# Kernel optimization log

Measured on AMD Instinct MI355X. Metric: run time of the kernel, lower is better.

## Reference

```python
import jax, jax.numpy as jnp
import numpy as np

# Problem sizes (see shape_source)
C = 4096                      # sparse matrix is C x C
NUMEL = C * C                 # 16,777,216
S = 3355443                   # round(NUMEL * 0.2) sampled gradient entries
R = 1048576                   # result_quantity (top-k buffer size)
DECAY = 0.95                  # decay_constant
FRAC = S / float(NUMEL)       # fractional_sparsity (mask_active=False branch)


def setup_inputs() -> dict:
    key = jax.random.key(0)
    k1, k2, k3, k4 = jax.random.split(key, 4)
    # Sampled linear indices into the C x C grid (forward: torch.randint(0, numel, [S]))
    sample_index = jax.random.randint(k1, (S,), 0, NUMEL, dtype=jnp.int32)
    # Steady-state buffer of (row, col) pairs and their running gradient magnitudes
    result_index = jax.random.randint(k2, (R, 2), 0, C, dtype=jnp.int32)
    result_value = jax.random.uniform(k3, (R,), dtype=jnp.float32)
    # Incoming gradient on the sampled accumulator entries
    gradient = jax.random.normal(k4, (S,), dtype=jnp.float32)
    return {
        "sample_index": sample_index,
        "result_index": result_index,
        "result_value": result_value,
        "gradient": gradient,
    }


def reference(sample_index, result_index, result_value, gradient):
    """Faithful JAX version of StochasticSubSampler's backward-hook update:
    decay the stored buffer, take |gradient| on the new samples, coalesce
    duplicated (row, col) entries by summation, then keep the top-R values.
    Returns (new_result_index [R,2] int32, new_result_value [R] float32)."""
    adj_decay = 1.0 - FRAC * (1.0 - DECAY)  # adjusted decay constant

    # Linearized keys for coalescing. sample_index is already row*C + col.
    samp_keys = sample_index
    res_keys = result_index[:, 0] * C + result_index[:, 1]
    keys = jnp.concatenate([samp_keys, res_keys])               # [K]
    vals = jnp.concatenate([jnp.abs(gradient), adj_decay * result_value])  # [K]
    K = keys.shape[0]

    # Coalesce: sum values that share the same (row, col) key.
    uniq, inv = jnp.unique(keys, size=K, fill_value=-1, return_inverse=True)
    summed = jax.ops.segment_sum(vals, inv, num_segments=K)     # [K]
    counts = jax.ops.segment_sum(jnp.ones_like(vals), inv, num_segments=K)
    neg = jnp.finfo(jnp.float32).min
    summed = jnp.where(counts > 0, summed, neg)  # mask padded unique slots

    # Descending sort + top-R selection (argsort(-v)[:R] in the original).
    top_vals, top_pos = jax.lax.top_k(summed, R)
    top_keys = uniq[top_pos]
    new_index = jnp.stack([top_keys // C, top_keys % C], axis=-1)  # [R, 2]
    return new_index, top_vals
```

## Files before the change

### kernel.cpp

```cpp
#include <hip/hip_runtime.h>
#include <stdint.h>

#define CDIM   4096
#define S_N    3355443
#define R_N    1048576
#define N1     (S_N + R_N)
#define TILE   4096
#define NTILES ((N1 + TILE - 1) / TILE)
#define NPAD   (NTILES * TILE)
#define NSB    (NPAD / 256)
#define PAD_KEY 0xFFFFFFu
#define PAD_VAL 0xFFFFFFFFu

static __device__ __forceinline__ unsigned blockScanExcl(unsigned v, unsigned t,
                                                         unsigned* lw, unsigned* tot){
  unsigned lane = t & 63u, w = t >> 6;
  unsigned x = v;
  #pragma unroll
  for (int off = 1; off < 64; off <<= 1){
    unsigned y = __shfl_up(x, off, 64);
    if (lane >= (unsigned)off) x += y;
  }
  if (lane == 63u) lw[w] = x;
  __syncthreads();
  unsigned woff = 0;
  for (unsigned i = 0; i < w; i++) woff += lw[i];
  *tot = lw[0] + lw[1] + lw[2] + lw[3];
  __syncthreads();
  return x + woff - v;
}

__global__ __launch_bounds__(256) void k_build(const int* __restrict__ sidx,
                                               const int* __restrict__ ridx,
                                               const float* __restrict__ rval,
                                               const float* __restrict__ grad,
                                               uint64_t* __restrict__ A){
  unsigned i = blockIdx.x * 256u + threadIdx.x;
  uint32_t key, vb;
  if (i < S_N){
    key = (uint32_t)sidx[i];
    vb  = __float_as_uint(fabsf(grad[i]));
  } else if (i < N1){
    unsigned j = i - S_N;
    key = (uint32_t)(ridx[2u*j] * CDIM + ridx[2u*j + 1u]);
    const float ADJF = (float)(1.0 - (3355443.0 / 16777216.0) * (1.0 - 0.95));
    vb = __float_as_uint(ADJF * rval[j]);
  } else {
    key = PAD_KEY; vb = PAD_VAL;
  }
  A[i] = ((uint64_t)key << 32) | (uint64_t)vb;
}

__global__ __launch_bounds__(256) void k_hist(const uint64_t* __restrict__ in, unsigned shift,
                                              unsigned* __restrict__ gh){
  __shared__ unsigned h[256];
  unsigned t = threadIdx.x;
  h[t] = 0; __syncthreads();
  size_t base = (size_t)blockIdx.x * TILE;
  #pragma unroll
  for (int r = 0; r < 16; r++){
    uint64_t e = in[base + (size_t)r*256 + t];
    atomicAdd(&h[(unsigned)((e >> shift) & 0xFF)], 1u);
  }
  __syncthreads();
  gh[t * NTILES + blockIdx.x] = h[t];
}

__global__ __launch_bounds__(256) void k_scanrows(unsigned* __restrict__ gh,
                                                  unsigned* __restrict__ dtot){
  __shared__ unsigned lw[4];
  unsigned d = blockIdx.x, t = threadIdx.x;
  unsigned carry = 0;
  for (unsigned base = 0; base < NTILES; base += 256){
    unsigned i = base + t;
    unsigned v = (i < NTILES) ? gh[d * NTILES + i] : 0u;
    unsigned tot;
    unsigned e = blockScanExcl(v, t, lw, &tot);
    if (i < NTILES) gh[d * NTILES + i] = e + carry;
    carry += tot;
  }
  if (t == 0) dtot[d] = carry;
}

template <bool FINAL>
__device__ __forceinline__ void scatter_body(const uint64_t* __restrict__ in,
                                             uint64_t* __restrict__ out,
                                             float* __restrict__ fout,
                                             unsigned shift,
                                             const unsigned* __restrict__ gh,
                                             const unsigned* __restrict__ dtot){
  __shared__ unsigned wrun[4*256];
  __shared__ unsigned gput[256];
  __shared__ unsigned lw[4];
  __shared__ uint64_t stage[TILE];
  unsigned t = threadIdx.x, lane = t & 63u, w = t >> 6;
  wrun[t] = 0; wrun[256+t] = 0; wrun[512+t] = 0; wrun[768+t] = 0;
  __syncthreads();
  uint64_t ltm = (lane == 0) ? 0ull : (~0ull >> (64u - lane));
  uint64_t elems[16]; unsigned rnk[16]; unsigned dg[16];
  size_t base = (size_t)blockIdx.x * TILE + (size_t)w * 1024;
  #pragma unroll
  for (int r = 0; r < 16; r++){
    uint64_t e = in[base + (size_t)r*64 + lane];
    elems[r] = e;
    unsigned d = (unsigned)((e >> shift) & 0xFF);
    uint64_t m = ~0ull;
    #pragma unroll
    for (int b = 0; b < 8; b++){
      uint64_t bb = __ballot((d >> b) & 1u);
      m &= ((d >> b) & 1u) ? bb : ~bb;
    }
    unsigned rr   = (unsigned)__popcll(m & ltm);
    unsigned prev = wrun[w*256 + d];
    __builtin_amdgcn_wave_barrier();
    if (rr == 0) wrun[w*256 + d] = prev + (unsigned)__popcll(m);
    __builtin_amdgcn_wave_barrier();
    rnk[r] = prev + rr;
    dg[r]  = d;
  }
  __syncthreads();
  {
    unsigned d = t;
    unsigned c0 = wrun[d], c1 = wrun[256+d], c2 = wrun[512+d], c3 = wrun[768+d];
    unsigned cnt = c0 + c1 + c2 + c3;
    unsigned tot;
    unsigned ldig  = blockScanExcl(cnt, t, lw, &tot);
    unsigned tot2;
    unsigned dbase = blockScanExcl(dtot[d], t, lw, &tot2);
    gput[d] = dbase + gh[d * NTILES + blockIdx.x] - ldig;
    wrun[d]       = ldig;
    wrun[256 + d] = ldig + c0;
    wrun[512 + d] = ldig + c0 + c1;
    wrun[768 + d] = ldig + c0 + c1 + c2;
  }
  __syncthreads();
  #pragma unroll
  for (int r = 0; r < 16; r++)
    stage[ wrun[w*256 + dg[r]] + rnk[r] ] = elems[r];
  __syncthreads();
  #pragma unroll
  for (int r = 0; r < 16; r++){
    unsigned j = (unsigned)r * 256u + t;
    uint64_t e = stage[j];
    unsigned d = (unsigned)((e >> shift) & 0xFF);
    unsigned dest = gput[d] + j;
    if (FINAL){
      if (dest < R_N){
        uint32_t key = (uint32_t)(e >> 32);
        fout[2u*dest]        = (float)(key >> 12);
        fout[2u*dest + 1u]   = (float)(key & 4095u);
        fout[2u*R_N + dest]  = __uint_as_float(~(uint32_t)e);
      }
    } else {
      out[dest] = e;
    }
  }
}

__global__ __launch_bounds__(256) void k_scatter(const uint64_t* __restrict__ in,
                                                 uint64_t* __restrict__ out,
                                                 unsigned shift,
                                                 const unsigned* __restrict__ gh,
                                                 const unsigned* __restrict__ dtot){
  scatter_body<false>(in, out, nullptr, shift, gh, dtot);
}

__global__ __launch_bounds__(256) void k_scatter_out(const uint64_t* __restrict__ in,
                                                     float* __restrict__ fout,
                                                     unsigned shift,
                                                     const unsigned* __restrict__ gh,
                                                     const unsigned* __restrict__ dtot){
  scatter_body<true>(in, nullptr, fout, shift, gh, dtot);
}

__global__ __launch_bounds__(256) void k_headcount(const uint64_t* __restrict__ in,
                                                   unsigned* __restrict__ hcnt){
  __shared__ unsigned wc[4];
  unsigned t = threadIdx.x, lane = t & 63u, w = t >> 6;
  size_t p = (size_t)blockIdx.x * 256 + t;
  uint64_t e = in[p];
  uint32_t k = (uint32_t)(e >> 32);
  bool head = ((p == 0) || ((uint32_t)(in[p-1] >> 32) != k)) && ((uint32_t)e != PAD_VAL);
  uint64_t m = __ballot(head);
  if (lane == 0) wc[w] = (unsigned)__popcll(m);
  __syncthreads();
  if (t == 0) hcnt[blockIdx.x] = wc[0] + wc[1] + wc[2] + wc[3];
}

__global__ __launch_bounds__(256) void k_scanheads(unsigned* __restrict__ hcnt,
                                                   unsigned* __restrict__ utot){
  __shared__ unsigned short buf[NSB];
  __shared__ unsigned lw[4];
  unsigned t = threadIdx.x;
  for (unsigned i = t; i < NSB; i += 256) buf[i] = (unsigned short)hcnt[i];
  __syncthreads();
  const unsigned CH = (NSB + 255) / 256;
  unsigned s = 0;
  for (unsigned k = 0; k < CH; k++){
    unsigned i = t * CH + k;
    if (i < NSB) s += buf[i];
  }
  unsigned tot;
  unsigned carry = blockScanExcl(s, t, lw, &tot);
  for (unsigned k = 0; k < CH; k++){
    unsigned i = t * CH + k;
    if (i < NSB){ unsigned v = buf[i]; hcnt[i] = carry; carry += v; }
  }
  if (t == 0) utot[0] = tot;
}

__global__ __launch_bounds__(256) void k_fill_tail(uint64_t* __restrict__ A,
                                                   const unsigned* __restrict__ utot){
  unsigned U = utot[0];
  unsigned i = blockIdx.x * 256u + threadIdx.x;
  if (i >= U) A[i] = ((uint64_t)PAD_KEY << 32) | (uint64_t)PAD_VAL;
}

__global__ __launch_bounds__(256) void k_segsum(const uint64_t* __restrict__ in,
                                                uint64_t* __restrict__ out,
                                                const unsigned* __restrict__ hbase){
  __shared__ unsigned wc[4], woffs[4];
  unsigned t = threadIdx.x, lane = t & 63u, w = t >> 6;
  size_t p = (size_t)blockIdx.x * 256 + t;
  uint64_t e0 = in[p];
  uint32_t k = (uint32_t)(e0 >> 32);
  bool head = ((p == 0) || ((uint32_t)(in[p-1] >> 32) != k)) && ((uint32_t)e0 != PAD_VAL);
  uint64_t m = __ballot(head);
  if (lane == 0) wc[w] = (unsigned)__popcll(m);
  __syncthreads();
  if (t == 0){ unsigned a = 0; for (int i = 0; i < 4; i++){ woffs[i] = a; a += wc[i]; } }
  __syncthreads();
  if (head){
    uint64_t ltm = (lane == 0) ? 0ull : (~0ull >> (64u - lane));
    unsigned rank = (unsigned)__popcll(m & ltm);
    unsigned oidx = hbase[blockIdx.x] + woffs[w] + rank;
    float s = __uint_as_float((uint32_t)e0);
    size_t q = p + 1;
    while (q < NPAD){
      uint64_t e = in[q];
      if ((uint32_t)(e >> 32) != k) break;
      uint32_t vb = (uint32_t)e;
      if (vb == PAD_VAL) break;
      s += __uint_as_float(vb);
      q++;
    }
    out[oidx] = ((uint64_t)k << 32) | (uint64_t)(uint32_t)(~__float_as_uint(s));
  }
}

extern "C" void kernel_launch(void* const* d_in, const int* in_sizes, int n_in,
                              void* d_out, int out_size, void* d_ws, size_t ws_size,
                              hipStream_t stream) {
  const int*   sidx = (const int*)d_in[0];
  const int*   ridx = (const int*)d_in[1];
  const float* rval = (const float*)d_in[2];
  const float* grad = (const float*)d_in[3];
  float* out = (float*)d_out;

  uint64_t* A0   = (uint64_t*)d_ws;
  uint64_t* A1   = A0 + NPAD;
  unsigned* gh   = (unsigned*)(A1 + NPAD);
  unsigned* dtot = gh + 256 * NTILES;
  unsigned* hcnt = dtot + 256;
  unsigned* utot = hcnt + NSB;

  k_build<<<NSB, 256, 0, stream>>>(sidx, ridx, rval, grad, A0);

  k_hist    <<<NTILES, 256, 0, stream>>>(A0, 32, gh);
  k_scanrows<<<256,    256, 0, stream>>>(gh, dtot);
  k_scatter <<<NTILES, 256, 0, stream>>>(A0, A1, 32, gh, dtot);
  k_hist    <<<NTILES, 256, 0, stream>>>(A1, 40, gh);
  k_scanrows<<<256,    256, 0, stream>>>(gh, dtot);
  k_scatter <<<NTILES, 256, 0, stream>>>(A1, A0, 40, gh, dtot);
  k_hist    <<<NTILES, 256, 0, stream>>>(A0, 48, gh);
  k_scanrows<<<256,    256, 0, stream>>>(gh, dtot);
  k_scatter <<<NTILES, 256, 0, stream>>>(A0, A1, 48, gh, dtot);

  k_headcount<<<NSB, 256, 0, stream>>>(A1, hcnt);
  k_scanheads<<<1,   256, 0, stream>>>(hcnt, utot);
  k_fill_tail<<<NSB, 256, 0, stream>>>(A0, utot);
  k_segsum   <<<NSB, 256, 0, stream>>>(A1, A0, hcnt);

  k_hist    <<<NTILES, 256, 0, stream>>>(A0, 0, gh);
  k_scanrows<<<256,    256, 0, stream>>>(gh, dtot);
  k_scatter <<<NTILES, 256, 0, stream>>>(A0, A1, 0, gh, dtot);
  k_hist    <<<NTILES, 256, 0, stream>>>(A1, 8, gh);
  k_scanrows<<<256,    256, 0, stream>>>(gh, dtot);
  k_scatter <<<NTILES, 256, 0, stream>>>(A1, A0, 8, gh, dtot);
  k_hist    <<<NTILES, 256, 0, stream>>>(A0, 16, gh);
  k_scanrows<<<256,    256, 0, stream>>>(gh, dtot);
  k_scatter <<<NTILES, 256, 0, stream>>>(A0, A1, 16, gh, dtot);
  k_hist       <<<NTILES, 256, 0, stream>>>(A1, 24, gh);
  k_scanrows   <<<256,    256, 0, stream>>>(gh, dtot);
  k_scatter_out<<<NTILES, 256, 0, stream>>>(A1, out, 24, gh, dtot);
}
```

Before: 433.4 us.

## Replace per-pass histogram/scan kernels with onesweep decoupled-lookback radix scatter

Global digit histograms for all passes are now computed up front: three key-digit histograms are fused into the build kernel and four value-digit histograms come from one extra kernel. Each scatter pass then derives its per-tile offsets through decoupled lookback on a status array, with tile order taken from a ticket counter and an epoch tag per pass. This removes one histogram kernel and one row-scan kernel per pass, along with a full read of the data for each histogram. In exchange it adds spin-waiting on inter-block status flags and global atomics.

```diff
diff --git a/kernel.cpp b/kernel.cpp
--- a/kernel.cpp
+++ b/kernel.cpp
@@ -11,6 +11,14 @@
 #define NSB    (NPAD / 256)
 #define PAD_KEY 0xFFFFFFu
 #define PAD_VAL 0xFFFFFFFFu
+#define VALMASK 0x07FFFFFFu
+
+static __device__ __forceinline__ unsigned ld_st(unsigned* p){
+  return __hip_atomic_load(p, __ATOMIC_RELAXED, __HIP_MEMORY_SCOPE_AGENT);
+}
+static __device__ __forceinline__ void st_st(unsigned* p, unsigned v){
+  __hip_atomic_store(p, v, __ATOMIC_RELAXED, __HIP_MEMORY_SCOPE_AGENT);
+}
 
 static __device__ __forceinline__ unsigned blockScanExcl(unsigned v, unsigned t,
                                                          unsigned* lw, unsigned* tot){
@@ -30,75 +38,92 @@
   return x + woff - v;
 }
 
-__global__ __launch_bounds__(256) void k_build(const int* __restrict__ sidx,
-                                               const int* __restrict__ ridx,
-                                               const float* __restrict__ rval,
-                                               const float* __restrict__ grad,
-                                               uint64_t* __restrict__ A){
+__global__ __launch_bounds__(256) void k_zero(unsigned* __restrict__ p, unsigned n){
   unsigned i = blockIdx.x * 256u + threadIdx.x;
-  uint32_t key, vb;
-  if (i < S_N){
-    key = (uint32_t)sidx[i];
-    vb  = __float_as_uint(fabsf(grad[i]));
-  } else if (i < N1){
-    unsigned j = i - S_N;
-    key = (uint32_t)(ridx[2u*j] * CDIM + ridx[2u*j + 1u]);
-    const float ADJF = (float)(1.0 - (3355443.0 / 16777216.0) * (1.0 - 0.95));
-    vb = __float_as_uint(ADJF * rval[j]);
-  } else {
-    key = PAD_KEY; vb = PAD_VAL;
-  }
-  A[i] = ((uint64_t)key << 32) | (uint64_t)vb;
-}
-
-__global__ __launch_bounds__(256) void k_hist(const uint64_t* __restrict__ in, unsigned shift,
-                                              unsigned* __restrict__ gh){
-  __shared__ unsigned h[256];
+  if (i < n) p[i] = 0u;
+}
+
+__global__ __launch_bounds__(256) void k_build_h3(const int* __restrict__ sidx,
+                                                  const int* __restrict__ ridx,
+                                                  const float* __restrict__ rval,
+                                                  const float* __restrict__ grad,
+                                                  uint64_t* __restrict__ A,
+                                                  unsigned* __restrict__ dtotAll){
+  __shared__ unsigned h[3*256];
   unsigned t = threadIdx.x;
-  h[t] = 0; __syncthreads();
+  h[t] = 0; h[256+t] = 0; h[512+t] = 0;
+  __syncthreads();
+  unsigned base = blockIdx.x * (unsigned)TILE;
+  #pragma unroll
+  for (int r = 0; r < 16; r++){
+    unsigned i = base + (unsigned)r*256u + t;
+    uint32_t key, vb;
+    if (i < S_N){
+      key = (uint32_t)sidx[i];
+      vb  = __float_as_uint(fabsf(grad[i]));
+    } else if (i < N1){
+      unsigned j = i - S_N;
+      key = (uint32_t)(ridx[2u*j] * CDIM + ridx[2u*j + 1u]);
+      const float ADJF = (float)(1.0 - (3355443.0 / 16777216.0) * (1.0 - 0.95));
+      vb = __float_as_uint(ADJF * rval[j]);
+    } else {
+      key = PAD_KEY; vb = PAD_VAL;
+    }
+    A[i] = ((uint64_t)key << 32) | (uint64_t)vb;
+    atomicAdd(&h[key & 0xFFu], 1u);
+    atomicAdd(&h[256u + ((key >> 8) & 0xFFu)], 1u);
+    atomicAdd(&h[512u + ((key >> 16) & 0xFFu)], 1u);
+  }
+  __syncthreads();
+  if (h[t])     atomicAdd(&dtotAll[t],        h[t]);
+  if (h[256+t]) atomicAdd(&dtotAll[256u + t], h[256+t]);
+  if (h[512+t]) atomicAdd(&dtotAll[512u + t], h[512+t]);
+}
+
+__global__ __launch_bounds__(256) void k_ghist4(const uint64_t* __restrict__ A,
+                                                unsigned* __restrict__ dtotAll){
+  __shared__ unsigned h[4*256];
+  unsigned t = threadIdx.x;
+  h[t] = 0; h[256+t] = 0; h[512+t] = 0; h[768+t] = 0;
+  __syncthreads();
   size_t base = (size_t)blockIdx.x * TILE;
   #pragma unroll
   for (int r = 0; r < 16; r++){
-    uint64_t e = in[base + (size_t)r*256 + t];
-    atomicAdd(&h[(unsigned)((e >> shift) & 0xFF)], 1u);
-  }
-  __syncthreads();
-  gh[t * NTILES + blockIdx.x] = h[t];
-}
-
-__global__ __launch_bounds__(256) void k_scanrows(unsigned* __restrict__ gh,
-                                                  unsigned* __restrict__ dtot){
-  __shared__ unsigned lw[4];
-  unsigned d = blockIdx.x, t = threadIdx.x;
-  unsigned carry = 0;
-  for (unsigned base = 0; base < NTILES; base += 256){
-    unsigned i = base + t;
-    unsigned v = (i < NTILES) ? gh[d * NTILES + i] : 0u;
-    unsigned tot;
-    unsigned e = blockScanExcl(v, t, lw, &tot);
-    if (i < NTILES) gh[d * NTILES + i] = e + carry;
-    carry += tot;
-  }
-  if (t == 0) dtot[d] = carry;
+    uint32_t x = (uint32_t)A[base + (size_t)r*256 + t];
+    atomicAdd(&h[x & 0xFFu], 1u);
+    atomicAdd(&h[256u + ((x >> 8)  & 0xFFu)], 1u);
+    atomicAdd(&h[512u + ((x >> 16) & 0xFFu)], 1u);
+    atomicAdd(&h[768u + (x >> 24)], 1u);
+  }
+  __syncthreads();
+  #pragma unroll
+  for (int rr = 0; rr < 4; rr++){
+    unsigned v = h[rr*256 + t];
+    if (v) atomicAdd(&dtotAll[(3u + rr)*256u + t], v);
+  }
 }
 
 template <bool FINAL>
-__device__ __forceinline__ void scatter_body(const uint64_t* __restrict__ in,
-                                             uint64_t* __restrict__ out,
-                                             float* __restrict__ fout,
-                                             unsigned shift,
-                                             const unsigned* __restrict__ gh,
-                                             const unsigned* __restrict__ dtot){
+__device__ __forceinline__ void scatter_os(const uint64_t* __restrict__ in,
+                                           uint64_t* __restrict__ out,
+                                           float* __restrict__ fout,
+                                           unsigned shift, unsigned epoch,
+                                           unsigned* __restrict__ status,
+                                           const unsigned* __restrict__ drow,
+                                           unsigned* __restrict__ ticket){
   __shared__ unsigned wrun[4*256];
   __shared__ unsigned gput[256];
   __shared__ unsigned lw[4];
+  __shared__ unsigned vts;
   __shared__ uint64_t stage[TILE];
   unsigned t = threadIdx.x, lane = t & 63u, w = t >> 6;
+  if (t == 0) vts = atomicAdd(ticket, 1u);
   wrun[t] = 0; wrun[256+t] = 0; wrun[512+t] = 0; wrun[768+t] = 0;
   __syncthreads();
+  unsigned vt = vts;
   uint64_t ltm = (lane == 0) ? 0ull : (~0ull >> (64u - lane));
   uint64_t elems[16]; unsigned rnk[16]; unsigned dg[16];
-  size_t base = (size_t)blockIdx.x * TILE + (size_t)w * 1024;
+  size_t base = (size_t)vt * TILE + (size_t)w * 1024;
   #pragma unroll
   for (int r = 0; r < 16; r++){
     uint64_t e = in[base + (size_t)r*64 + lane];
@@ -119,20 +144,45 @@
     dg[r]  = d;
   }
   __syncthreads();
-  {
-    unsigned d = t;
-    unsigned c0 = wrun[d], c1 = wrun[256+d], c2 = wrun[512+d], c3 = wrun[768+d];
-    unsigned cnt = c0 + c1 + c2 + c3;
-    unsigned tot;
-    unsigned ldig  = blockScanExcl(cnt, t, lw, &tot);
-    unsigned tot2;
-    unsigned dbase = blockScanExcl(dtot[d], t, lw, &tot2);
-    gput[d] = dbase + gh[d * NTILES + blockIdx.x] - ldig;
-    wrun[d]       = ldig;
-    wrun[256 + d] = ldig + c0;
-    wrun[512 + d] = ldig + c0 + c1;
-    wrun[768 + d] = ldig + c0 + c1 + c2;
-  }
+  unsigned d = t;
+  unsigned c0 = wrun[d], c1 = wrun[256+d], c2 = wrun[512+d], c3 = wrun[768+d];
+  unsigned cnt = c0 + c1 + c2 + c3;
+  if (vt == 0) st_st(&status[d],            (epoch << 29) | (2u << 27) | cnt);
+  else         st_st(&status[vt*256u + d],  (epoch << 29) | (1u << 27) | cnt);
+  unsigned tot, tot2;
+  unsigned ldig  = blockScanExcl(cnt, t, lw, &tot);
+  unsigned dbase = blockScanExcl(drow[d], t, lw, &tot2);
+  unsigned excl = 0;
+  if (vt){
+    int j = (int)vt - 1;
+    unsigned running = 0;
+    bool fin = false;
+    while (!fin){
+      int nb = (j >= 3) ? 4 : (j + 1);
+      unsigned wv[4];
+      #pragma unroll
+      for (int b = 0; b < 4; b++)
+        if (b < nb) wv[b] = ld_st(&status[(unsigned)(j - b)*256u + d]);
+      #pragma unroll
+      for (int b = 0; b < 4; b++){
+        if (b < nb && !fin){
+          unsigned x = wv[b];
+          while ((x >> 29) != epoch || !((x >> 27) & 3u))
+            x = ld_st(&status[(unsigned)(j - b)*256u + d]);
+          running += x & VALMASK;
+          if (((x >> 27) & 3u) == 2u) fin = true;
+        }
+      }
+      if (!fin){ j -= nb; if (j < 0) fin = true; }
+    }
+    excl = running;
+    st_st(&status[vt*256u + d], (epoch << 29) | (2u << 27) | (excl + cnt));
+  }
+  gput[d] = dbase + excl - ldig;
+  wrun[d]       = ldig;
+  wrun[256 + d] = ldig + c0;
+  wrun[512 + d] = ldig + c0 + c1;
+  wrun[768 + d] = ldig + c0 + c1 + c2;
   __syncthreads();
   #pragma unroll
   for (int r = 0; r < 16; r++)
@@ -140,10 +190,10 @@
   __syncthreads();
   #pragma unroll
   for (int r = 0; r < 16; r++){
-    unsigned j = (unsigned)r * 256u + t;
-    uint64_t e = stage[j];
-    unsigned d = (unsigned)((e >> shift) & 0xFF);
-    unsigned dest = gput[d] + j;
+    unsigned jj = (unsigned)r * 256u + t;
+    uint64_t e = stage[jj];
+    unsigned dd = (unsigned)((e >> shift) & 0xFF);
+    unsigned dest = gput[dd] + jj;
     if (FINAL){
       if (dest < R_N){
         uint32_t key = (uint32_t)(e >> 32);
@@ -157,20 +207,22 @@
   }
 }
 
-__global__ __launch_bounds__(256) void k_scatter(const uint64_t* __restrict__ in,
-                                                 uint64_t* __restrict__ out,
-                                                 unsigned shift,
-                                                 const unsigned* __restrict__ gh,
-                                                 const unsigned* __restrict__ dtot){
-  scatter_body<false>(in, out, nullptr, shift, gh, dtot);
-}
-
-__global__ __launch_bounds__(256) void k_scatter_out(const uint64_t* __restrict__ in,
-                                                     float* __restrict__ fout,
-                                                     unsigned shift,
-                                                     const unsigned* __restrict__ gh,
-                                                     const unsigned* __restrict__ dtot){
-  scatter_body<true>(in, nullptr, fout, shift, gh, dtot);
+__global__ __launch_bounds__(256) void k_scat(const uint64_t* __restrict__ in,
+                                              uint64_t* __restrict__ out,
+                                              unsigned shift, unsigned epoch,
+                                              unsigned* __restrict__ status,
+                                              const unsigned* __restrict__ drow,
+                                              unsigned* __restrict__ ticket){
+  scatter_os<false>(in, out, nullptr, shift, epoch, status, drow, ticket);
+}
+
+__global__ __launch_bounds__(256) void k_scat_out(const uint64_t* __restrict__ in,
+                                                  float* __restrict__ fout,
+                                                  unsigned shift, unsigned epoch,
+                                                  unsigned* __restrict__ status,
+                                                  const unsigned* __restrict__ drow,
+                                                  unsigned* __restrict__ ticket){
+  scatter_os<true>(in, nullptr, fout, shift, epoch, status, drow, ticket);
 }
 
 __global__ __launch_bounds__(256) void k_headcount(const uint64_t* __restrict__ in,
@@ -257,40 +309,31 @@
   const float* grad = (const float*)d_in[3];
   float* out = (float*)d_out;
 
-  uint64_t* A0   = (uint64_t*)d_ws;
-  uint64_t* A1   = A0 + NPAD;
-  unsigned* gh   = (unsigned*)(A1 + NPAD);
-  unsigned* dtot = gh + 256 * NTILES;
-  unsigned* hcnt = dtot + 256;
-  unsigned* utot = hcnt + NSB;
-
-  k_build<<<NSB, 256, 0, stream>>>(sidx, ridx, rval, grad, A0);
-
-  k_hist    <<<NTILES, 256, 0, stream>>>(A0, 32, gh);
-  k_scanrows<<<256,    256, 0, stream>>>(gh, dtot);
-  k_scatter <<<NTILES, 256, 0, stream>>>(A0, A1, 32, gh, dtot);
-  k_hist    <<<NTILES, 256, 0, stream>>>(A1, 40, gh);
-  k_scanrows<<<256,    256, 0, stream>>>(gh, dtot);
-  k_scatter <<<NTILES, 256, 0, stream>>>(A1, A0, 40, gh, dtot);
-  k_hist    <<<NTILES, 256, 0, stream>>>(A0, 48, gh);
-  k_scanrows<<<256,    256, 0, stream>>>(gh, dtot);
-  k_scatter <<<NTILES, 256, 0, stream>>>(A0, A1, 48, gh, dtot);
+  uint64_t* A0      = (uint64_t*)d_ws;
+  uint64_t* A1      = A0 + NPAD;
+  unsigned* status  = (unsigned*)(A1 + NPAD);
+  unsigned* dtotAll = status + NTILES*256;
+  unsigned* tickets = dtotAll + 7*256;
+  unsigned* hcnt    = tickets + 8;
+  unsigned* utot    = hcnt + NSB;
+
+  const unsigned NZ = NTILES*256 + 7*256 + 8;
+  k_zero<<<(NZ + 255)/256, 256, 0, stream>>>(status, NZ);
+
+  k_build_h3<<<NTILES, 256, 0, stream>>>(sidx, ridx, rval, grad, A0, dtotAll);
+
+  k_scat<<<NTILES, 256, 0, stream>>>(A0, A1, 32, 1, status, dtotAll + 0*256, tickets + 0);
+  k_scat<<<NTILES, 256, 0, stream>>>(A1, A0, 40, 2, status, dtotAll + 1*256, tickets + 1);
+  k_scat<<<NTILES, 256, 0, stream>>>(A0, A1, 48, 3, status, dtotAll + 2*256, tickets + 2);
 
   k_headcount<<<NSB, 256, 0, stream>>>(A1, hcnt);
   k_scanheads<<<1,   256, 0, stream>>>(hcnt, utot);
   k_fill_tail<<<NSB, 256, 0, stream>>>(A0, utot);
   k_segsum   <<<NSB, 256, 0, stream>>>(A1, A0, hcnt);
 
-  k_hist    <<<NTILES, 256, 0, stream>>>(A0, 0, gh);
-  k_scanrows<<<256,    256, 0, stream>>>(gh, dtot);
-  k_scatter <<<NTILES, 256, 0, stream>>>(A0, A1, 0, gh, dtot);
-  k_hist    <<<NTILES, 256, 0, stream>>>(A1, 8, gh);
-  k_scanrows<<<256,    256, 0, stream>>>(gh, dtot);
-  k_scatter <<<NTILES, 256, 0, stream>>>(A1, A0, 8, gh, dtot);
-  k_hist    <<<NTILES, 256, 0, stream>>>(A0, 16, gh);
-  k_scanrows<<<256,    256, 0, stream>>>(gh, dtot);
-  k_scatter <<<NTILES, 256, 0, stream>>>(A0, A1, 16, gh, dtot);
-  k_hist       <<<NTILES, 256, 0, stream>>>(A1, 24, gh);
-  k_scanrows   <<<256,    256, 0, stream>>>(gh, dtot);
-  k_scatter_out<<<NTILES, 256, 0, stream>>>(A1, out, 24, gh, dtot);
-}
+  k_ghist4<<<NTILES, 256, 0, stream>>>(A0, dtotAll);
+  k_scat    <<<NTILES, 256, 0, stream>>>(A0, A1,  0, 4, status, dtotAll + 3*256, tickets + 3);
+  k_scat    <<<NTILES, 256, 0, stream>>>(A1, A0,  8, 5, status, dtotAll + 4*256, tickets + 4);
+  k_scat    <<<NTILES, 256, 0, stream>>>(A0, A1, 16, 6, status, dtotAll + 5*256, tickets + 5);
+  k_scat_out<<<NTILES, 256, 0, stream>>>(A1, out, 24, 7, status, dtotAll + 6*256, tickets + 6);
+}
```

After: 587.7 us. 1.36x slower.

## Prefilter top-R candidates by 16-bit value threshold before final radix sort

Applied to the files above, without the earlier changes.

After segment-sum, the code builds a histogram of the top value bits, picks a 16-bit threshold that keeps at least R entries, and compacts only those candidates into a buffer of about 1.3M slots. The four value radix passes then run over that small buffer instead of the full 4.4M array. This cuts most of the final sort traffic but adds histogram, count, scan and compact kernels, plus global atomics. It also relies on the candidates above the threshold fitting in the fixed padded buffer.

```diff
diff --git a/kernel.cpp b/kernel.cpp
--- a/kernel.cpp
+++ b/kernel.cpp
@@ -9,6 +9,8 @@
 #define NTILES ((N1 + TILE - 1) / TILE)
 #define NPAD   (NTILES * TILE)
 #define NSB    (NPAD / 256)
+#define NT2    320
+#define SPAD   (NT2 * TILE)
 #define PAD_KEY 0xFFFFFFu
 #define PAD_VAL 0xFFFFFFFFu
 
@@ -28,6 +30,11 @@
   *tot = lw[0] + lw[1] + lw[2] + lw[3];
   __syncthreads();
   return x + woff - v;
+}
+
+__global__ __launch_bounds__(256) void k_zero(unsigned* __restrict__ p, unsigned n){
+  unsigned i = blockIdx.x * 256u + threadIdx.x;
+  if (i < n) p[i] = 0u;
 }
 
 __global__ __launch_bounds__(256) void k_build(const int* __restrict__ sidx,
@@ -52,7 +59,7 @@
 }
 
 __global__ __launch_bounds__(256) void k_hist(const uint64_t* __restrict__ in, unsigned shift,
-                                              unsigned* __restrict__ gh){
+                                              unsigned* __restrict__ gh, unsigned nt){
   __shared__ unsigned h[256];
   unsigned t = threadIdx.x;
   h[t] = 0; __syncthreads();
@@ -63,20 +70,20 @@
     atomicAdd(&h[(unsigned)((e >> shift) & 0xFF)], 1u);
   }
   __syncthreads();
-  gh[t * NTILES + blockIdx.x] = h[t];
+  gh[t * nt + blockIdx.x] = h[t];
 }
 
 __global__ __launch_bounds__(256) void k_scanrows(unsigned* __restrict__ gh,
-                                                  unsigned* __restrict__ dtot){
+                                                  unsigned* __restrict__ dtot, unsigned nt){
   __shared__ unsigned lw[4];
   unsigned d = blockIdx.x, t = threadIdx.x;
   unsigned carry = 0;
-  for (unsigned base = 0; base < NTILES; base += 256){
+  for (unsigned base = 0; base < nt; base += 256){
     unsigned i = base + t;
-    unsigned v = (i < NTILES) ? gh[d * NTILES + i] : 0u;
+    unsigned v = (i < nt) ? gh[d * nt + i] : 0u;
     unsigned tot;
     unsigned e = blockScanExcl(v, t, lw, &tot);
-    if (i < NTILES) gh[d * NTILES + i] = e + carry;
+    if (i < nt) gh[d * nt + i] = e + carry;
     carry += tot;
   }
   if (t == 0) dtot[d] = carry;
@@ -88,7 +95,8 @@
                                              float* __restrict__ fout,
                                              unsigned shift,
                                              const unsigned* __restrict__ gh,
-                                             const unsigned* __restrict__ dtot){
+                                             const unsigned* __restrict__ dtot,
+                                             unsigned nt){
   __shared__ unsigned wrun[4*256];
   __shared__ unsigned gput[256];
   __shared__ unsigned lw[4];
@@ -123,11 +131,10 @@
     unsigned d = t;
     unsigned c0 = wrun[d], c1 = wrun[256+d], c2 = wrun[512+d], c3 = wrun[768+d];
     unsigned cnt = c0 + c1 + c2 + c3;
-    unsigned tot;
+    unsigned tot, tot2;
     unsigned ldig  = blockScanExcl(cnt, t, lw, &tot);
-    unsigned tot2;
     unsigned dbase = blockScanExcl(dtot[d], t, lw, &tot2);
-    gput[d] = dbase + gh[d * NTILES + blockIdx.x] - ldig;
+    gput[d] = dbase + gh[d * nt + blockIdx.x] - ldig;
     wrun[d]       = ldig;
     wrun[256 + d] = ldig + c0;
     wrun[512 + d] = ldig + c0 + c1;
@@ -161,16 +168,18 @@
                                                  uint64_t* __restrict__ out,
                                                  unsigned shift,
                                                  const unsigned* __restrict__ gh,
-                                                 const unsigned* __restrict__ dtot){
-  scatter_body<false>(in, out, nullptr, shift, gh, dtot);
+                                                 const unsigned* __restrict__ dtot,
+                                                 unsigned nt){
+  scatter_body<false>(in, out, nullptr, shift, gh, dtot, nt);
 }
 
 __global__ __launch_bounds__(256) void k_scatter_out(const uint64_t* __restrict__ in,
                                                      float* __restrict__ fout,
                                                      unsigned shift,
                                                      const unsigned* __restrict__ gh,
-                                                     const unsigned* __restrict__ dtot){
-  scatter_body<true>(in, nullptr, fout, shift, gh, dtot);
+                                                     const unsigned* __restrict__ dtot,
+                                                     unsigned nt){
+  scatter_body<true>(in, nullptr, fout, shift, gh, dtot, nt);
 }
 
 __global__ __launch_bounds__(256) void k_headcount(const uint64_t* __restrict__ in,
@@ -218,9 +227,12 @@
 
 __global__ __launch_bounds__(256) void k_segsum(const uint64_t* __restrict__ in,
                                                 uint64_t* __restrict__ out,
-                                                const unsigned* __restrict__ hbase){
+                                                const unsigned* __restrict__ hbase,
+                                                unsigned* __restrict__ h_hi){
   __shared__ unsigned wc[4], woffs[4];
+  __shared__ unsigned hh[256];
   unsigned t = threadIdx.x, lane = t & 63u, w = t >> 6;
+  hh[t] = 0;
   size_t p = (size_t)blockIdx.x * 256 + t;
   uint64_t e0 = in[p];
   uint32_t k = (uint32_t)(e0 >> 32);
@@ -244,7 +256,95 @@
       s += __uint_as_float(vb);
       q++;
     }
-    out[oidx] = ((uint64_t)k << 32) | (uint64_t)(uint32_t)(~__float_as_uint(s));
+    uint32_t sk = ~__float_as_uint(s);
+    out[oidx] = ((uint64_t)k << 32) | (uint64_t)sk;
+    atomicAdd(&hh[sk >> 24], 1u);
+  }
+  __syncthreads();
+  if (hh[t]) atomicAdd(&h_hi[t], hh[t]);
+}
+
+static __device__ __forceinline__ unsigned pick_hi(const unsigned* h_hi, unsigned* cumExcl){
+  unsigned cum = 0;
+  for (unsigned b = 0; b < 256; b++){
+    unsigned c = h_hi[b];
+    if (cum + c >= R_N){ *cumExcl = cum; return b; }
+    cum += c;
+  }
+  *cumExcl = cum; return 255u;
+}
+static __device__ __forceinline__ unsigned pick_thr16(const unsigned* h_hi,
+                                                      const unsigned* h_lo){
+  unsigned cumB;
+  unsigned b = pick_hi(h_hi, &cumB);
+  unsigned cum = cumB;
+  for (unsigned c = 0; c < 256; c++){
+    unsigned v = h_lo[c];
+    if (cum + v >= R_N) return (b << 8) | c;
+    cum += v;
+  }
+  return (b << 8) | 255u;
+}
+
+__global__ __launch_bounds__(256) void k_selhist_lo(const uint64_t* __restrict__ A,
+                                                    const unsigned* __restrict__ h_hi,
+                                                    unsigned* __restrict__ h_lo){
+  __shared__ unsigned h[256];
+  __shared__ unsigned bstar;
+  unsigned t = threadIdx.x;
+  h[t] = 0;
+  if (t == 0){ unsigned dummy; bstar = pick_hi(h_hi, &dummy); }
+  __syncthreads();
+  unsigned bs = bstar;
+  size_t base = (size_t)blockIdx.x * TILE;
+  #pragma unroll
+  for (int r = 0; r < 16; r++){
+    uint32_t vb = (uint32_t)A[base + (size_t)r*256 + t];
+    if ((vb >> 24) == bs) atomicAdd(&h[(vb >> 16) & 0xFFu], 1u);
+  }
+  __syncthreads();
+  if (h[t]) atomicAdd(&h_lo[t], h[t]);
+}
+
+__global__ __launch_bounds__(256) void k_cmpcount(const uint64_t* __restrict__ A,
+                                                  const unsigned* __restrict__ h_hi,
+                                                  const unsigned* __restrict__ h_lo,
+                                                  unsigned* __restrict__ ccnt){
+  __shared__ unsigned wc[4];
+  __shared__ unsigned thr;
+  unsigned t = threadIdx.x, lane = t & 63u, w = t >> 6;
+  if (t == 0) thr = pick_thr16(h_hi, h_lo);
+  __syncthreads();
+  size_t p = (size_t)blockIdx.x * 256 + t;
+  bool q = (((uint32_t)A[p]) >> 16) <= thr;
+  uint64_t m = __ballot(q);
+  if (lane == 0) wc[w] = (unsigned)__popcll(m);
+  __syncthreads();
+  if (t == 0) ccnt[blockIdx.x] = wc[0] + wc[1] + wc[2] + wc[3];
+}
+
+__global__ __launch_bounds__(256) void k_compact(const uint64_t* __restrict__ A,
+                                                 uint64_t* __restrict__ B,
+                                                 const unsigned* __restrict__ h_hi,
+                                                 const unsigned* __restrict__ h_lo,
+                                                 const unsigned* __restrict__ cbase){
+  __shared__ unsigned wc[4], woffs[4];
+  __shared__ unsigned thr;
+  unsigned t = threadIdx.x, lane = t & 63u, w = t >> 6;
+  if (t == 0) thr = pick_thr16(h_hi, h_lo);
+  __syncthreads();
+  size_t p = (size_t)blockIdx.x * 256 + t;
+  uint64_t e = A[p];
+  bool q = (((uint32_t)e) >> 16) <= thr;
+  uint64_t m = __ballot(q);
+  if (lane == 0) wc[w] = (unsigned)__popcll(m);
+  __syncthreads();
+  if (t == 0){ unsigned a = 0; for (int i = 0; i < 4; i++){ woffs[i] = a; a += wc[i]; } }
+  __syncthreads();
+  if (q){
+    uint64_t ltm = (lane == 0) ? 0ull : (~0ull >> (64u - lane));
+    unsigned rank = (unsigned)__popcll(m & ltm);
+    B[cbase[blockIdx.x] + woffs[w] + rank] = e;
   }
 }
 
@@ -263,34 +363,45 @@
   unsigned* dtot = gh + 256 * NTILES;
   unsigned* hcnt = dtot + 256;
   unsigned* utot = hcnt + NSB;
-
+  unsigned* h_hi = utot + 1;
+  unsigned* h_lo = h_hi + 256;
+  unsigned* ccnt = h_lo + 256;
+  unsigned* mtot = ccnt + NSB;
+
+  k_zero <<<2, 256, 0, stream>>>(h_hi, 512);
   k_build<<<NSB, 256, 0, stream>>>(sidx, ridx, rval, grad, A0);
 
-  k_hist    <<<NTILES, 256, 0, stream>>>(A0, 32, gh);
-  k_scanrows<<<256,    256, 0, stream>>>(gh, dtot);
-  k_scatter <<<NTILES, 256, 0, stream>>>(A0, A1, 32, gh, dtot);
-  k_hist    <<<NTILES, 256, 0, stream>>>(A1, 40, gh);
-  k_scanrows<<<256,    256, 0, stream>>>(gh, dtot);
-  k_scatter <<<NTILES, 256, 0, stream>>>(A1, A0, 40, gh, dtot);
-  k_hist    <<<NTILES, 256, 0, stream>>>(A0, 48, gh);
-  k_scanrows<<<256,    256, 0, stream>>>(gh, dtot);
-  k_scatter <<<NTILES, 256, 0, stream>>>(A0, A1, 48, gh, dtot);
+  k_hist    <<<NTILES, 256, 0, stream>>>(A0, 32, gh, NTILES);
+  k_scanrows<<<256,    256, 0, stream>>>(gh, dtot, NTILES);
+  k_scatter <<<NTILES, 256, 0, stream>>>(A0, A1, 32, gh, dtot, NTILES);
+  k_hist    <<<NTILES, 256, 0, stream>>>(A1, 40, gh, NTILES);
+  k_scanrows<<<256,    256, 0, stream>>>(gh, dtot, NTILES);
+  k_scatter <<<NTILES, 256, 0, stream>>>(A1, A0, 40, gh, dtot, NTILES);
+  k_hist    <<<NTILES, 256, 0, stream>>>(A0, 48, gh, NTILES);
+  k_scanrows<<<256,    256, 0, stream>>>(gh, dtot, NTILES);
+  k_scatter <<<NTILES, 256, 0, stream>>>(A0, A1, 48, gh, dtot, NTILES);
 
   k_headcount<<<NSB, 256, 0, stream>>>(A1, hcnt);
   k_scanheads<<<1,   256, 0, stream>>>(hcnt, utot);
   k_fill_tail<<<NSB, 256, 0, stream>>>(A0, utot);
-  k_segsum   <<<NSB, 256, 0, stream>>>(A1, A0, hcnt);
-
-  k_hist    <<<NTILES, 256, 0, stream>>>(A0, 0, gh);
-  k_scanrows<<<256,    256, 0, stream>>>(gh, dtot);
-  k_scatter <<<NTILES, 256, 0, stream>>>(A0, A1, 0, gh, dtot);
-  k_hist    <<<NTILES, 256, 0, stream>>>(A1, 8, gh);
-  k_scanrows<<<256,    256, 0, stream>>>(gh, dtot);
-  k_scatter <<<NTILES, 256, 0, stream>>>(A1, A0, 8, gh, dtot);
-  k_hist    <<<NTILES, 256, 0, stream>>>(A0, 16, gh);
-  k_scanrows<<<256,    256, 0, stream>>>(gh, dtot);
-  k_scatter <<<NTILES, 256, 0, stream>>>(A0, A1, 16, gh, dtot);
-  k_hist       <<<NTILES, 256, 0, stream>>>(A1, 24, gh);
-  k_scanrows   <<<256,    256, 0, stream>>>(gh, dtot);
-  k_scatter_out<<<NTILES, 256, 0, stream>>>(A1, out, 24, gh, dtot);
-}
+  k_segsum   <<<NSB, 256, 0, stream>>>(A1, A0, hcnt, h_hi);
+
+  k_selhist_lo<<<NTILES, 256, 0, stream>>>(A0, h_hi, h_lo);
+  k_cmpcount  <<<NSB, 256, 0, stream>>>(A0, h_hi, h_lo, ccnt);
+  k_scanheads <<<1,   256, 0, stream>>>(ccnt, mtot);
+  k_compact   <<<NSB, 256, 0, stream>>>(A0, A1, h_hi, h_lo, ccnt);
+  k_fill_tail <<<SPAD/256, 256, 0, stream>>>(A1, mtot);
+
+  k_hist    <<<NT2, 256, 0, stream>>>(A1, 0, gh, NT2);
+  k_scanrows<<<256, 256, 0, stream>>>(gh, dtot, NT2);
+  k_scatter <<<NT2, 256, 0, stream>>>(A1, A0, 0, gh, dtot, NT2);
+  k_hist    <<<NT2, 256, 0, stream>>>(A0, 8, gh, NT2);
+  k_scanrows<<<256, 256, 0, stream>>>(gh, dtot, NT2);
+  k_scatter <<<NT2, 256, 0, stream>>>(A0, A1, 8, gh, dtot, NT2);
+  k_hist    <<<NT2, 256, 0, stream>>>(A1, 16, gh, NT2);
+  k_scanrows<<<256, 256, 0, stream>>>(gh, dtot, NT2);
+  k_scatter <<<NT2, 256, 0, stream>>>(A1, A0, 16, gh, dtot, NT2);
+  k_hist       <<<NT2, 256, 0, stream>>>(A0, 24, gh, NT2);
+  k_scanrows   <<<256, 256, 0, stream>>>(gh, dtot, NT2);
+  k_scatter_out<<<NT2, 256, 0, stream>>>(A0, out, 24, gh, dtot, NT2);
+}
```

New measurement: 1.121 ms. 159% more time.
